# Performance work log

Hardware: AMD Instinct MI355X
Metric: run time of the kernel (lower is better)

## Reference

```python
import jax, jax.numpy as jnp
import numpy as np

HIDDEN = 4096
HEADS = 32
HEAD_DIM = HIDDEN // HEADS  # 128; kv length must equal this (additive-bias broadcast)
B, SQ, SK = 4, 2048, HEAD_DIM


def _split_heads(x):
    # [B, T, HIDDEN] -> [B, H, T, d]
    b, t, _ = x.shape
    return x.reshape(b, t, HEADS, HEAD_DIM).transpose(0, 2, 1, 3)


def setup_inputs() -> dict:
    key = jax.random.key(0)
    ks = jax.random.split(key, 8)
    s = 1.0 / np.sqrt(HIDDEN)
    return {
        "q": jax.random.normal(ks[0], (B, SQ, HIDDEN), jnp.float32),
        "k": jax.random.normal(ks[1], (B, SK, HIDDEN), jnp.float32),
        "v": jax.random.normal(ks[2], (B, SK, HIDDEN), jnp.float32),
        "r": jax.random.normal(ks[3], (B, SQ, HIDDEN), jnp.float32),
        "Wq": jax.random.normal(ks[4], (HIDDEN, HIDDEN), jnp.float32) * s,
        "Wk": jax.random.normal(ks[5], (HIDDEN, HIDDEN), jnp.float32) * s,
        "Wv": jax.random.normal(ks[6], (HIDDEN, HIDDEN), jnp.float32) * s,
        "Wo": jax.random.normal(ks[7], (HIDDEN, HIDDEN), jnp.float32) * s,
    }


def reference(q, k, v, r, Wq, Wk, Wv, Wo):
    qh = _split_heads(q @ Wq)           # [B,H,SQ,d]
    kh = _split_heads(k @ Wk)           # [B,H,SK,d]
    vh = _split_heads(v @ Wv)           # [B,H,SK,d]
    rh = _split_heads(r @ Wo)           # [B,H,SQ,d] ; d == SK, added as bias
    scale = 1.0 / np.sqrt(HEAD_DIM).astype(np.float32)
    scores = jnp.einsum("bhqd,bhkd->bhqk", qh, kh) * scale + rh
    attn = jax.nn.softmax(scores, axis=-1)
    ctx = jnp.einsum("bhqk,bhkd->bhqd", attn, vh)       # [B,H,SQ,d]
    ctx = ctx.transpose(0, 2, 1, 3).reshape(q.shape[0], -1, HIDDEN)
    return ctx @ Wo  # Wo reused for output projection, as in source
```

## Files before the change

kernel.cpp:

```cpp
#include <hip/hip_runtime.h>
#include <hip/hip_bf16.h>

typedef unsigned short u16;
typedef unsigned int   u32;
typedef unsigned long long u64;
typedef __attribute__((ext_vector_type(8))) short short8;
typedef __attribute__((ext_vector_type(4))) float f32x4;

#define HID   4096
#define NHEAD 32
#define HD    128
#define NB    4
#define NSQ   2048
#define NSK   128
#define MROWS (NB*NSQ)
#define KROWS (NB*NSK)

__device__ __forceinline__ u16 f2bf(float f) {
  u32 u = __builtin_bit_cast(u32, f);
  u += 0x7fffu + ((u >> 16) & 1u);
  return (u16)(u >> 16);
}

__device__ __forceinline__ u64 pack4(float4 f) {
  return (u64)f2bf(f.x) | ((u64)f2bf(f.y) << 16) |
         ((u64)f2bf(f.z) << 32) | ((u64)f2bf(f.w) << 48);
}

__device__ __forceinline__ uint4 packu16x8(const u16* v) {
  uint4 o;
  o.x = (u32)v[0] | ((u32)v[1] << 16);
  o.y = (u32)v[2] | ((u32)v[3] << 16);
  o.z = (u32)v[4] | ((u32)v[5] << 16);
  o.w = (u32)v[6] | ((u32)v[7] << 16);
  return o;
}

__device__ __forceinline__ f32x4 mfma16(short8 a, short8 b, f32x4 c) {
  return __builtin_amdgcn_mfma_f32_16x16x32_bf16(a, b, c, 0, 0, 0);
}

__device__ __forceinline__ void gload_lds16(const u16* g, u16* l) {
  __builtin_amdgcn_global_load_lds((const __attribute__((address_space(1))) u32*)g,
                                   (__attribute__((address_space(3))) u32*)l, 16, 0, 0);
}

__global__ __launch_bounds__(256) void convert_bf16_x2(const float* __restrict__ in0,
                                                       u16* __restrict__ out0,
                                                       const float* __restrict__ in1,
                                                       u16* __restrict__ out1, long long n4)
{
  const float* in = blockIdx.y ? in1 : in0;
  u16* out = blockIdx.y ? out1 : out0;
  long long i = (long long)blockIdx.x * blockDim.x + threadIdx.x;
  const long long stride = (long long)gridDim.x * blockDim.x;
  for (; i < n4; i += stride) {
    float4 f = ((const float4*)in)[i];
    ((u64*)out)[i] = pack4(f);
  }
}

__global__ __launch_bounds__(256) void transpose_convert_x4(const float* __restrict__ W0, u16* __restrict__ T0,
                                                            const float* __restrict__ W1, u16* __restrict__ T1,
                                                            const float* __restrict__ W2, u16* __restrict__ T2,
                                                            const float* __restrict__ W3, u16* __restrict__ T3)
{
  const int z = blockIdx.z;
  const float* W = (z == 0) ? W0 : (z == 1) ? W1 : (z == 2) ? W2 : W3;
  u16* Wt = (z == 0) ? T0 : (z == 1) ? T1 : (z == 2) ? T2 : T3;
  __shared__ __align__(16) u16 tile[64][72];
  const int t = threadIdx.x;
  const int c0 = blockIdx.x * 64, r0 = blockIdx.y * 64;
  #pragma unroll
  for (int i = 0; i < 4; ++i) {
    int e = i * 1024 + t * 4;
    int rr = e >> 6, cc = e & 63;
    float4 f = *(const float4*)(W + (size_t)(r0 + rr) * HID + c0 + cc);
    *(u64*)&tile[rr][cc] = pack4(f);
  }
  __syncthreads();
  #pragma unroll
  for (int i = 0; i < 2; ++i) {
    int e = i * 2048 + t * 8;
    int cc = e >> 6, rr = e & 63;
    u16 vals[8];
    #pragma unroll
    for (int jj = 0; jj < 8; ++jj) vals[jj] = tile[rr + jj][cc];
    *(uint4*)(Wt + (size_t)(c0 + cc) * HID + r0 + rr) = packu16x8(vals);
  }
}

__global__ __launch_bounds__(256) void transpose_head(const u16* __restrict__ Vh,
                                                      u16* __restrict__ VT)
{
  __shared__ __align__(16) u16 tile[128][136];
  const int t = threadIdx.x;
  const int bh = blockIdx.x;
  const int b = bh >> 5, h = bh & 31;
  #pragma unroll
  for (int i = 0; i < 8; ++i) {
    int e = i * 2048 + t * 8;
    int tr = e >> 7, d = e & 127;
    *(uint4*)&tile[tr][d] = *(const uint4*)(Vh + ((size_t)b * NSK + tr) * HID + h * HD + d);
  }
  __syncthreads();
  #pragma unroll
  for (int i = 0; i < 8; ++i) {
    int e = i * 2048 + t * 8;
    int d = e >> 7, tt = e & 127;
    u16 vals[8];
    #pragma unroll
    for (int jj = 0; jj < 8; ++jj) vals[jj] = tile[tt + jj][d];
    *(uint4*)(VT + ((size_t)bh * HD + d) * NSK + tt) = packu16x8(vals);
  }
}


__device__ __forceinline__ short8 ldf(const u16* buf, int r, int cb) {
  return *(const short8*)(buf + r * 64 + (cb ^ ((r & 7) << 3)));
}

__device__ __forceinline__ void stage2(u16* dst, const u16* g, long off0, long off1, int tid) {
  gload_lds16(g + off0, dst + tid * 8);
  gload_lds16(g + off1, dst + 4096 + tid * 8);
}

#define BAR() do { __builtin_amdgcn_sched_barrier(0); __builtin_amdgcn_s_barrier(); \
                   __builtin_amdgcn_sched_barrier(0); } while (0)

#define MFMA16(R0, AV, BV) do { \
  __builtin_amdgcn_s_setprio(1); \
  _Pragma("unroll") \
  for (int _i = 0; _i < 4; ++_i) \
    _Pragma("unroll") \
    for (int _j = 0; _j < 4; ++_j) \
      acc[(R0) + _i][_j] = mfma16(AV[_i], BV[_j], acc[(R0) + _i][_j]); \
  __builtin_amdgcn_s_setprio(0); \
} while (0)

template<int VM, bool S1, bool S2, bool NEXT>
__device__ __forceinline__ void tile4p(const u16* __restrict__ Ag, const u16* __restrict__ Bg,
                                       int kt, u16* Ac, u16* Bc, u16* Ao, u16* Bo,
                                       int wm, int wn, int g8, int c16,
                                       long off0, long off1, int tid,
                                       short8 (&afA)[4], short8 (&afB)[4],
                                       short8 (&bfA)[4], short8 (&bfB)[4],
                                       f32x4 (&acc)[8][4])
{
  #pragma unroll
  for (int i = 0; i < 4; ++i) afB[i] = ldf(Ac, wm * 128 + 64 + i * 16 + c16, g8);
  if constexpr (S1) stage2(Ao + 8192, Ag + (size_t)128 * HID + kt + 64, off0, off1, tid);
  BAR();
  MFMA16(0, afA, bfA);

  #pragma unroll
  for (int i = 0; i < 4; ++i) afA[i] = ldf(Ac, wm * 128 + i * 16 + c16, 32 + g8);
  #pragma unroll
  for (int j = 0; j < 4; ++j) bfB[j] = ldf(Bc, wn * 64 + j * 16 + c16, 32 + g8);
  if constexpr (S1) stage2(Bo + 8192, Bg + (size_t)128 * HID + kt + 64, off0, off1, tid);
  BAR();
  MFMA16(4, afB, bfA);

  #pragma unroll
  for (int i = 0; i < 4; ++i) afB[i] = ldf(Ac, wm * 128 + 64 + i * 16 + c16, 32 + g8);
  if constexpr (S2) stage2(Bc, Bg + kt + 128, off0, off1, tid);
  BAR();
  MFMA16(0, afA, bfB);

  if constexpr (S2) stage2(Ac, Ag + kt + 128, off0, off1, tid);
  if constexpr (VM >= 0) asm volatile("s_waitcnt vmcnt(%0)" :: "n"(VM) : "memory");
  BAR();
  if constexpr (NEXT) {
    #pragma unroll
    for (int i = 0; i < 4; ++i) afA[i] = ldf(Ao, wm * 128 + i * 16 + c16, g8);
    #pragma unroll
    for (int j = 0; j < 4; ++j) bfA[j] = ldf(Bo, wn * 64 + j * 16 + c16, g8);
  }
  MFMA16(4, afB, bfB);
}

template<bool OUTF32, bool EXTRA>
__global__ __launch_bounds__(512, 2) void gemm256(const u16* __restrict__ A,
                                                  const u16* __restrict__ Bt,
                                                  void* __restrict__ Cv,
                                                  const u16* __restrict__ A2,
                                                  const u16* __restrict__ BtK,
                                                  const u16* __restrict__ BtV,
                                                  u16* __restrict__ KhO,
                                                  u16* __restrict__ VhO)
{
  __shared__ __align__(16) u16 As[2][16384];
  __shared__ __align__(16) u16 Bs[2][16384];
  const int tid = threadIdx.x;
  const int l = tid & 63, wv = tid >> 6;
  const int g8 = (l >> 4 & 3) * 8, c16 = l & 15;
  const int g = l >> 4 & 3;
  const int wm = wv >> 2, wn = wv & 3;

  const int nwg = gridDim.x;
  int wg = blockIdx.x;
  wg = (wg & 7) * (nwg >> 3) + (wg >> 3);

  const u16* Ag; const u16* Bg; u16* Ch = nullptr; float* Cf = nullptr; int n0;
  if constexpr (EXTRA) {
    if (wg >= 512) {
      const int e = wg - 512, mt = e >> 4;
      n0 = (e & 15) * 256;
      Ag = A2 + (size_t)(mt << 8) * HID;
      Bg = (mt < 2 ? BtK : BtV) + (size_t)n0 * HID;
      Ch = (mt < 2 ? KhO : VhO) + (size_t)((mt & 1) << 8) * HID;
    } else {
      const int m0 = (wg >> 4) * 256; n0 = (wg & 15) * 256;
      Ag = A + (size_t)m0 * HID;
      Bg = Bt + (size_t)n0 * HID;
      Ch = (u16*)Cv + (size_t)m0 * HID;
    }
  } else {
    const int m0 = (wg >> 4) * 256; n0 = (wg & 15) * 256;
    Ag = A + (size_t)m0 * HID;
    Bg = Bt + (size_t)n0 * HID;
    if constexpr (OUTF32) Cf = (float*)Cv + (size_t)m0 * HID;
    else                  Ch = (u16*)Cv + (size_t)m0 * HID;
  }

  const long off0 = (long)(tid >> 3) * HID + (((tid & 7) ^ ((tid >> 3) & 7)) * 8);
  const long off1 = off0 + (long)64 * HID;

  f32x4 acc[8][4] = {};
  short8 afA[4], afB[4], bfA[4], bfB[4];

  stage2(&Bs[0][0],    Bg,                     off0, off1, tid);
  stage2(&As[0][0],    Ag,                     off0, off1, tid);
  stage2(&As[0][8192], Ag + (size_t)128 * HID, off0, off1, tid);
  stage2(&Bs[0][8192], Bg + (size_t)128 * HID, off0, off1, tid);
  stage2(&Bs[1][0],    Bg + 64,                off0, off1, tid);
  stage2(&As[1][0],    Ag + 64,                off0, off1, tid);
  asm volatile("s_waitcnt vmcnt(4)" ::: "memory");
  BAR();
  #pragma unroll
  for (int i = 0; i < 4; ++i) afA[i] = ldf(&As[0][0], wm * 128 + i * 16 + c16, g8);
  #pragma unroll
  for (int j = 0; j < 4; ++j) bfA[j] = ldf(&Bs[0][0], wn * 64 + j * 16 + c16, g8);

  constexpr int NT = HID / 64;
  for (int T = 0; T < NT - 2; T += 2) {
    tile4p<4, true, true, true>(Ag, Bg, T * 64,      &As[0][0], &Bs[0][0], &As[1][0], &Bs[1][0],
                                wm, wn, g8, c16, off0, off1, tid, afA, afB, bfA, bfB, acc);
    tile4p<4, true, true, true>(Ag, Bg, T * 64 + 64, &As[1][0], &Bs[1][0], &As[0][0], &Bs[0][0],
                                wm, wn, g8, c16, off0, off1, tid, afA, afB, bfA, bfB, acc);
  }
  tile4p<0, true, false, true>(Ag, Bg, (NT - 2) * 64, &As[0][0], &Bs[0][0], &As[1][0], &Bs[1][0],
                               wm, wn, g8, c16, off0, off1, tid, afA, afB, bfA, bfB, acc);
  tile4p<-1, false, false, false>(Ag, Bg, (NT - 1) * 64, &As[1][0], &Bs[1][0], &As[0][0], &Bs[0][0],
                                  wm, wn, g8, c16, off0, off1, tid, afA, afB, bfA, bfB, acc);

  #pragma unroll
  for (int mi = 0; mi < 8; ++mi)
    #pragma unroll
    for (int j = 0; j < 4; ++j)
      #pragma unroll
      for (int rr = 0; rr < 4; ++rr) {
        const size_t idx = (size_t)(wm * 128 + mi * 16 + g * 4 + rr) * HID
                         + n0 + wn * 64 + j * 16 + c16;
        if constexpr (OUTF32) Cf[idx] = acc[mi][j][rr];
        else                  Ch[idx] = f2bf(acc[mi][j][rr]);
      }
}

__global__ __launch_bounds__(256) void attn_kernel(const u16*  __restrict__ Qh,
                                                   const u16*  __restrict__ Kh,
                                                   const u16*  __restrict__ VT,
                                                   const float* __restrict__ Rh,
                                                   u16* __restrict__ ctx)
{
  __shared__ __align__(16) u16 Plds[4][32][136];
  const int t = threadIdx.x;
  const int w = t >> 6, l = t & 63;
  const int g = l >> 4, c = l & 15;
  const int qc = blockIdx.x;
  const int bh = blockIdx.y;
  const int b = bh >> 5, h = bh & 31;
  const size_t qrow0 = (size_t)b * NSQ + qc * 128 + w * 32;
  const float SCALE = 0.08838834764831845f;

  f32x4 s[2][8] = {};
  #pragma unroll
  for (int ks = 0; ks < 4; ++ks) {
    const int ko = ks * 32 + g * 8;
    short8 af[2];
    #pragma unroll
    for (int i = 0; i < 2; ++i)
      af[i] = *(const short8*)(Qh + (qrow0 + i * 16 + c) * HID + h * HD + ko);
    #pragma unroll
    for (int j = 0; j < 8; ++j) {
      short8 bfr = *(const short8*)(Kh + ((size_t)b * NSK + j * 16 + c) * HID + h * HD + ko);
      s[0][j] = mfma16(af[0], bfr, s[0][j]);
      s[1][j] = mfma16(af[1], bfr, s[1][j]);
    }
  }

  float rinv[2][4];
  #pragma unroll
  for (int i = 0; i < 2; ++i) {
    #pragma unroll
    for (int rr = 0; rr < 4; ++rr) {
      const size_t qr = qrow0 + i * 16 + g * 4 + rr;
      float vmax = -3.0e38f;
      #pragma unroll
      for (int j = 0; j < 8; ++j) {
        float bias = Rh[qr * HID + h * HD + j * 16 + c];
        float sv = s[i][j][rr] * SCALE + bias;
        s[i][j][rr] = sv;
        vmax = fmaxf(vmax, sv);
      }
      #pragma unroll
      for (int m = 1; m < 16; m <<= 1) vmax = fmaxf(vmax, __shfl_xor(vmax, m));
      float ssum = 0.f;
      #pragma unroll
      for (int j = 0; j < 8; ++j) {
        float p = __expf(s[i][j][rr] - vmax);
        s[i][j][rr] = p;
        ssum += p;
      }
      #pragma unroll
      for (int m = 1; m < 16; m <<= 1) ssum += __shfl_xor(ssum, m);
      rinv[i][rr] = 1.f / ssum;
    }
  }

  #pragma unroll
  for (int i = 0; i < 2; ++i)
    #pragma unroll
    for (int j = 0; j < 8; ++j)
      #pragma unroll
      for (int rr = 0; rr < 4; ++rr)
        Plds[w][i * 16 + g * 4 + rr][j * 16 + c] = f2bf(s[i][j][rr]);
  __syncthreads();

  #pragma unroll
  for (int i = 0; i < 2; ++i) {
    f32x4 o[8] = {};
    #pragma unroll
    for (int ks = 0; ks < 4; ++ks) {
      const int ko = ks * 32 + g * 8;
      short8 pa = *(const short8*)(&Plds[w][i * 16 + c][ko]);
      #pragma unroll
      for (int j = 0; j < 8; ++j) {
        short8 bv = *(const short8*)(VT + ((size_t)bh * HD + j * 16 + c) * NSK + ko);
        o[j] = mfma16(pa, bv, o[j]);
      }
    }
    #pragma unroll
    for (int j = 0; j < 8; ++j)
      #pragma unroll
      for (int rr = 0; rr < 4; ++rr) {
        const size_t row = qrow0 + i * 16 + g * 4 + rr;
        ctx[row * HID + h * HD + j * 16 + c] = f2bf(o[j][rr] * rinv[i][rr]);
      }
  }
}

extern "C" void kernel_launch(void* const* d_in, const int* in_sizes, int n_in,
                              void* d_out, int out_size, void* d_ws, size_t ws_size,
                              hipStream_t stream)
{
  const float* q  = (const float*)d_in[0];
  const float* k  = (const float*)d_in[1];
  const float* v  = (const float*)d_in[2];
  const float* r  = (const float*)d_in[3];
  const float* Wq = (const float*)d_in[4];
  const float* Wk = (const float*)d_in[5];
  const float* Wv = (const float*)d_in[6];
  const float* Wo = (const float*)d_in[7];
  float* out = (float*)d_out;

  char* ws = (char*)d_ws;
  #define WSMB(x) ((size_t)(x) << 20)
  u16* WoT = (u16*)(ws + WSMB(0));
  u16* Qh  = (u16*)(ws + WSMB(32));
  u16* Kh  = (u16*)(ws + WSMB(96));
  u16* Vh  = (u16*)(ws + WSMB(100));
  u16* VTb = (u16*)(ws + WSMB(104));
  u16* rb  = (u16*)(ws + WSMB(108));
  u16* ctx = (u16*)(ws + WSMB(108));
  u16* Sb  = (u16*)(ws + WSMB(172));
  u16* WqT = (u16*)(ws + WSMB(236));
  u16* WkT = (u16*)((char*)d_out + WSMB(0));
  u16* WvT = (u16*)((char*)d_out + WSMB(32));
  u16* kb  = (u16*)((char*)d_out + WSMB(64));
  u16* vb  = (u16*)((char*)d_out + WSMB(68));
  const size_t needed = WSMB(268);
  if (ws_size < needed) return;

  dim3 tb(256);
  dim3 tb5(512);
  const long long nBig = (long long)MROWS * HID / 4;
  const long long nSm  = (long long)KROWS * HID / 4;

  transpose_convert_x4<<<dim3(64, 64, 4), tb, 0, stream>>>(Wo, WoT, Wq, WqT, Wk, WkT, Wv, WvT);
  convert_bf16_x2<<<dim3(512, 2), tb, 0, stream>>>(k, kb, v, vb, nSm);
  convert_bf16_x2<<<dim3(2048, 2), tb, 0, stream>>>(q, Sb, r, rb, nBig);

  gemm256<false, true><<<dim3(576), tb5, 0, stream>>>(Sb, WqT, (void*)Qh,
                                                      kb, WkT, WvT, Kh, Vh);

  gemm256<true, false><<<dim3(512), tb5, 0, stream>>>(rb, WoT, (void*)out,
                                                      nullptr, nullptr, nullptr, nullptr, nullptr);

  transpose_head<<<dim3(128), tb, 0, stream>>>(Vh, VTb);

  attn_kernel<<<dim3(16, 128), tb, 0, stream>>>(Qh, Kh, VTb, out, ctx);

  gemm256<true, false><<<dim3(512), tb5, 0, stream>>>(ctx, WoT, (void*)out,
                                                      nullptr, nullptr, nullptr, nullptr, nullptr);
}
```

Baseline: 1.175 ms.

## Restructure GEMM k-tile schedule and store bias projection as bf16

The GEMM inner tile is rewritten to load A/B fragments from LDS in split groups just before each MFMA quarter, with explicit lgkmcnt waits. This replaces the earlier scheme that prefetched the next tile's fragments across iterations. Separately, the r@Wo bias projection is written as bf16 into the reused Sb buffer instead of fp32 into the output, and the attention kernel reads it as bf16. That halves the bias write and read traffic, at the cost of rounding the additive bias to bf16. Dropping the cross-tile fragment prefetch may expose LDS latency before the MFMAs.

```diff
diff --git a/kernel.cpp b/kernel.cpp
--- a/kernel.cpp
+++ b/kernel.cpp
@@ -22,6 +22,11 @@
   return (u16)(u >> 16);
 }
 
+__device__ __forceinline__ float bf2f(u16 x) {
+  u32 u = (u32)x << 16;
+  return __builtin_bit_cast(float, u);
+}
+
 __device__ __forceinline__ u64 pack4(float4 f) {
   return (u64)f2bf(f.x) | ((u64)f2bf(f.y) << 16) |
          ((u64)f2bf(f.z) << 32) | ((u64)f2bf(f.w) << 48);
@@ -125,58 +130,95 @@
   gload_lds16(g + off1, dst + 4096 + tid * 8);
 }
 
-#define BAR() do { __builtin_amdgcn_sched_barrier(0); __builtin_amdgcn_s_barrier(); \
-                   __builtin_amdgcn_sched_barrier(0); } while (0)
-
-#define MFMA16(R0, AV, BV) do { \
-  __builtin_amdgcn_s_setprio(1); \
-  _Pragma("unroll") \
-  for (int _i = 0; _i < 4; ++_i) \
-    _Pragma("unroll") \
-    for (int _j = 0; _j < 4; ++_j) \
-      acc[(R0) + _i][_j] = mfma16(AV[_i], BV[_j], acc[(R0) + _i][_j]); \
-  __builtin_amdgcn_s_setprio(0); \
-} while (0)
-
-template<int VM, bool S1, bool S2, bool NEXT>
-__device__ __forceinline__ void tile4p(const u16* __restrict__ Ag, const u16* __restrict__ Bg,
-                                       int kt, u16* Ac, u16* Bc, u16* Ao, u16* Bo,
-                                       int wm, int wn, int g8, int c16,
-                                       long off0, long off1, int tid,
-                                       short8 (&afA)[4], short8 (&afB)[4],
-                                       short8 (&bfA)[4], short8 (&bfB)[4],
-                                       f32x4 (&acc)[8][4])
-{
-  #pragma unroll
-  for (int i = 0; i < 4; ++i) afB[i] = ldf(Ac, wm * 128 + 64 + i * 16 + c16, g8);
+template<int VM, bool S1, bool S2>
+__device__ __forceinline__ void tile4(const u16* __restrict__ Ag, const u16* __restrict__ Bg,
+                                      int kt, u16* Ac, u16* Bc, u16* Ao, u16* Bo,
+                                      int wm, int wn, int g, int c16,
+                                      long off0, long off1, int tid, f32x4 (&acc)[8][4])
+{
+  const int g8 = g * 8;
+  short8 af[4][2], bf[4][2];
+
+  #pragma unroll
+  for (int i = 0; i < 4; ++i) {
+    const int r = wm * 128 + i * 16 + c16;
+    af[i][0] = ldf(Ac, r, g8); af[i][1] = ldf(Ac, r, 32 + g8);
+  }
+  #pragma unroll
+  for (int j = 0; j < 2; ++j) {
+    const int r = wn * 64 + j * 16 + c16;
+    bf[j][0] = ldf(Bc, r, g8); bf[j][1] = ldf(Bc, r, 32 + g8);
+  }
   if constexpr (S1) stage2(Ao + 8192, Ag + (size_t)128 * HID + kt + 64, off0, off1, tid);
-  BAR();
-  MFMA16(0, afA, bfA);
-
-  #pragma unroll
-  for (int i = 0; i < 4; ++i) afA[i] = ldf(Ac, wm * 128 + i * 16 + c16, 32 + g8);
-  #pragma unroll
-  for (int j = 0; j < 4; ++j) bfB[j] = ldf(Bc, wn * 64 + j * 16 + c16, 32 + g8);
+  asm volatile("s_waitcnt lgkmcnt(8)" ::: "memory");
+  __builtin_amdgcn_s_barrier();
+  asm volatile("s_waitcnt lgkmcnt(0)" ::: "memory");
+  __builtin_amdgcn_sched_barrier(0);
+  __builtin_amdgcn_s_setprio(1);
+  #pragma unroll
+  for (int i = 0; i < 4; ++i)
+    #pragma unroll
+    for (int j = 0; j < 2; ++j) {
+      acc[i][j] = mfma16(af[i][0], bf[j][0], acc[i][j]);
+      acc[i][j] = mfma16(af[i][1], bf[j][1], acc[i][j]);
+    }
+  __builtin_amdgcn_s_setprio(0);
+
+  #pragma unroll
+  for (int j = 2; j < 4; ++j) {
+    const int r = wn * 64 + j * 16 + c16;
+    bf[j][0] = ldf(Bc, r, g8); bf[j][1] = ldf(Bc, r, 32 + g8);
+  }
   if constexpr (S1) stage2(Bo + 8192, Bg + (size_t)128 * HID + kt + 64, off0, off1, tid);
-  BAR();
-  MFMA16(4, afB, bfA);
-
-  #pragma unroll
-  for (int i = 0; i < 4; ++i) afB[i] = ldf(Ac, wm * 128 + 64 + i * 16 + c16, 32 + g8);
+  __builtin_amdgcn_s_barrier();
+  asm volatile("s_waitcnt lgkmcnt(0)" ::: "memory");
+  __builtin_amdgcn_sched_barrier(0);
+  __builtin_amdgcn_s_setprio(1);
+  #pragma unroll
+  for (int i = 0; i < 4; ++i)
+    #pragma unroll
+    for (int j = 2; j < 4; ++j) {
+      acc[i][j] = mfma16(af[i][0], bf[j][0], acc[i][j]);
+      acc[i][j] = mfma16(af[i][1], bf[j][1], acc[i][j]);
+    }
+  __builtin_amdgcn_s_setprio(0);
+
+  #pragma unroll
+  for (int i = 0; i < 4; ++i) {
+    const int r = wm * 128 + 64 + i * 16 + c16;
+    af[i][0] = ldf(Ac, r, g8); af[i][1] = ldf(Ac, r, 32 + g8);
+  }
   if constexpr (S2) stage2(Bc, Bg + kt + 128, off0, off1, tid);
-  BAR();
-  MFMA16(0, afA, bfB);
+  __builtin_amdgcn_s_barrier();
+  asm volatile("s_waitcnt lgkmcnt(0)" ::: "memory");
+  __builtin_amdgcn_sched_barrier(0);
+  __builtin_amdgcn_s_setprio(1);
+  #pragma unroll
+  for (int i = 0; i < 4; ++i)
+    #pragma unroll
+    for (int j = 0; j < 2; ++j) {
+      acc[4 + i][j] = mfma16(af[i][0], bf[j][0], acc[4 + i][j]);
+      acc[4 + i][j] = mfma16(af[i][1], bf[j][1], acc[4 + i][j]);
+    }
+  __builtin_amdgcn_s_setprio(0);
 
   if constexpr (S2) stage2(Ac, Ag + kt + 128, off0, off1, tid);
-  if constexpr (VM >= 0) asm volatile("s_waitcnt vmcnt(%0)" :: "n"(VM) : "memory");
-  BAR();
-  if constexpr (NEXT) {
-    #pragma unroll
-    for (int i = 0; i < 4; ++i) afA[i] = ldf(Ao, wm * 128 + i * 16 + c16, g8);
-    #pragma unroll
-    for (int j = 0; j < 4; ++j) bfA[j] = ldf(Bo, wn * 64 + j * 16 + c16, g8);
-  }
-  MFMA16(4, afB, bfB);
+  if constexpr (VM == 4) {
+    asm volatile("s_waitcnt vmcnt(4)" ::: "memory");
+  } else if constexpr (VM == 0) {
+    asm volatile("s_waitcnt vmcnt(0)" ::: "memory");
+  }
+  __builtin_amdgcn_s_barrier();
+  __builtin_amdgcn_sched_barrier(0);
+  __builtin_amdgcn_s_setprio(1);
+  #pragma unroll
+  for (int i = 0; i < 4; ++i)
+    #pragma unroll
+    for (int j = 2; j < 4; ++j) {
+      acc[4 + i][j] = mfma16(af[i][0], bf[j][0], acc[4 + i][j]);
+      acc[4 + i][j] = mfma16(af[i][1], bf[j][1], acc[4 + i][j]);
+    }
+  __builtin_amdgcn_s_setprio(0);
 }
 
 template<bool OUTF32, bool EXTRA>
@@ -193,8 +235,7 @@
   __shared__ __align__(16) u16 Bs[2][16384];
   const int tid = threadIdx.x;
   const int l = tid & 63, wv = tid >> 6;
-  const int g8 = (l >> 4 & 3) * 8, c16 = l & 15;
-  const int g = l >> 4 & 3;
+  const int g = l >> 4 & 3, c16 = l & 15;
   const int wm = wv >> 2, wn = wv & 3;
 
   const int nwg = gridDim.x;
@@ -227,7 +268,6 @@
   const long off1 = off0 + (long)64 * HID;
 
   f32x4 acc[8][4] = {};
-  short8 afA[4], afB[4], bfA[4], bfB[4];
 
   stage2(&Bs[0][0],    Bg,                     off0, off1, tid);
   stage2(&As[0][0],    Ag,                     off0, off1, tid);
@@ -236,23 +276,20 @@
   stage2(&Bs[1][0],    Bg + 64,                off0, off1, tid);
   stage2(&As[1][0],    Ag + 64,                off0, off1, tid);
   asm volatile("s_waitcnt vmcnt(4)" ::: "memory");
-  BAR();
-  #pragma unroll
-  for (int i = 0; i < 4; ++i) afA[i] = ldf(&As[0][0], wm * 128 + i * 16 + c16, g8);
-  #pragma unroll
-  for (int j = 0; j < 4; ++j) bfA[j] = ldf(&Bs[0][0], wn * 64 + j * 16 + c16, g8);
+  __builtin_amdgcn_sched_barrier(0);
+  __builtin_amdgcn_s_barrier();
 
   constexpr int NT = HID / 64;
-  for (int T = 0; T < NT - 2; T += 2) {
-    tile4p<4, true, true, true>(Ag, Bg, T * 64,      &As[0][0], &Bs[0][0], &As[1][0], &Bs[1][0],
-                                wm, wn, g8, c16, off0, off1, tid, afA, afB, bfA, bfB, acc);
-    tile4p<4, true, true, true>(Ag, Bg, T * 64 + 64, &As[1][0], &Bs[1][0], &As[0][0], &Bs[0][0],
-                                wm, wn, g8, c16, off0, off1, tid, afA, afB, bfA, bfB, acc);
-  }
-  tile4p<0, true, false, true>(Ag, Bg, (NT - 2) * 64, &As[0][0], &Bs[0][0], &As[1][0], &Bs[1][0],
-                               wm, wn, g8, c16, off0, off1, tid, afA, afB, bfA, bfB, acc);
-  tile4p<-1, false, false, false>(Ag, Bg, (NT - 1) * 64, &As[1][0], &Bs[1][0], &As[0][0], &Bs[0][0],
-                                  wm, wn, g8, c16, off0, off1, tid, afA, afB, bfA, bfB, acc);
+  for (int T = 0; T < NT - 3; T += 2) {
+    tile4<4, true, true>(Ag, Bg, T * 64,      &As[0][0], &Bs[0][0], &As[1][0], &Bs[1][0],
+                         wm, wn, g, c16, off0, off1, tid, acc);
+    tile4<4, true, true>(Ag, Bg, T * 64 + 64, &As[1][0], &Bs[1][0], &As[0][0], &Bs[0][0],
+                         wm, wn, g, c16, off0, off1, tid, acc);
+  }
+  tile4<0, true, false>(Ag, Bg, (NT - 2) * 64, &As[0][0], &Bs[0][0], &As[1][0], &Bs[1][0],
+                        wm, wn, g, c16, off0, off1, tid, acc);
+  tile4<-1, false, false>(Ag, Bg, (NT - 1) * 64, &As[1][0], &Bs[1][0], &As[0][0], &Bs[0][0],
+                          wm, wn, g, c16, off0, off1, tid, acc);
 
   #pragma unroll
   for (int mi = 0; mi < 8; ++mi)
@@ -270,7 +307,7 @@
 __global__ __launch_bounds__(256) void attn_kernel(const u16*  __restrict__ Qh,
                                                    const u16*  __restrict__ Kh,
                                                    const u16*  __restrict__ VT,
-                                                   const float* __restrict__ Rh,
+                                                   const u16*  __restrict__ Rhb,
                                                    u16* __restrict__ ctx)
 {
   __shared__ __align__(16) u16 Plds[4][32][136];
@@ -308,7 +345,7 @@
       float vmax = -3.0e38f;
       #pragma unroll
       for (int j = 0; j < 8; ++j) {
-        float bias = Rh[qr * HID + h * HD + j * 16 + c];
+        float bias = bf2f(Rhb[qr * HID + h * HD + j * 16 + c]);
         float sv = s[i][j][rr] * SCALE + bias;
         s[i][j][rr] = sv;
         vmax = fmaxf(vmax, sv);
@@ -404,12 +441,12 @@
   gemm256<false, true><<<dim3(576), tb5, 0, stream>>>(Sb, WqT, (void*)Qh,
                                                       kb, WkT, WvT, Kh, Vh);
 
-  gemm256<true, false><<<dim3(512), tb5, 0, stream>>>(rb, WoT, (void*)out,
-                                                      nullptr, nullptr, nullptr, nullptr, nullptr);
+  gemm256<false, false><<<dim3(512), tb5, 0, stream>>>(rb, WoT, (void*)Sb,
+                                                       nullptr, nullptr, nullptr, nullptr, nullptr);
 
   transpose_head<<<dim3(128), tb, 0, stream>>>(Vh, VTb);
 
-  attn_kernel<<<dim3(16, 128), tb, 0, stream>>>(Qh, Kh, VTb, out, ctx);
+  attn_kernel<<<dim3(16, 128), tb, 0, stream>>>(Qh, Kh, VTb, Sb, ctx);
 
   gemm256<true, false><<<dim3(512), tb5, 0, stream>>>(ctx, WoT, (void*)out,
                                                       nullptr, nullptr, nullptr, nullptr, nullptr);
```

Result: faster. 1.110 ms (-5.6%).
